# Performance work log

Hardware: AMD Instinct MI355X
Metric: run time of the kernel (lower is better)

## Reference

```python
import jax, jax.numpy as jnp
import numpy as np


def _cayley():
    """8x8x8 structure constants of Cl(3,0): (a*b)[r] = sum_pq a[p] b[q] C[p,q,r].
    Built by evaluating the original geometric_product formulas on basis one-hots."""
    C = np.zeros((8, 8, 8), dtype=np.float32)
    for p in range(8):
        a = np.zeros(8, dtype=np.float32); a[p] = 1.0
        for q in range(8):
            b = np.zeros(8, dtype=np.float32); b[q] = 1.0
            C[p, q] = [
                a[0]*b[0] + a[1]*b[1] + a[2]*b[2] + a[3]*b[3] - a[4]*b[4] - a[5]*b[5] - a[6]*b[6] - a[7]*b[7],
                a[0]*b[1] + a[1]*b[0] - a[2]*b[4] - a[3]*b[5] + a[4]*b[2] + a[5]*b[3] - a[6]*b[7] - a[7]*b[6],
                a[0]*b[2] + a[1]*b[4] + a[2]*b[0] - a[3]*b[6] - a[4]*b[1] + a[5]*b[7] + a[6]*b[3] + a[7]*b[5],
                a[0]*b[3] + a[1]*b[5] + a[2]*b[6] + a[3]*b[0] - a[4]*b[7] - a[5]*b[1] - a[6]*b[2] - a[7]*b[4],
                a[0]*b[4] + a[1]*b[2] - a[2]*b[1] + a[3]*b[7] + a[4]*b[0] - a[5]*b[6] + a[6]*b[5] + a[7]*b[3],
                a[0]*b[5] + a[1]*b[3] - a[2]*b[7] - a[3]*b[1] + a[4]*b[6] + a[5]*b[0] - a[6]*b[4] - a[7]*b[2],
                a[0]*b[6] + a[1]*b[7] + a[2]*b[3] - a[3]*b[2] - a[4]*b[5] + a[5]*b[4] + a[6]*b[0] + a[7]*b[1],
                a[0]*b[7] + a[1]*b[6] - a[2]*b[5] + a[3]*b[4] + a[4]*b[3] - a[5]*b[2] + a[6]*b[1] + a[7]*b[0],
            ]
    return C

_C = jnp.asarray(_cayley())  # [8,8,8]

BATCH, IN_F, OUT_F = 4096, 512, 512


def setup_inputs() -> dict:
    key = jax.random.key(0)
    k1, k2, k3 = jax.random.split(key, 3)
    return {
        "x": jax.random.normal(k1, (BATCH, IN_F, 8), dtype=jnp.float32),
        "weight": jax.random.normal(k2, (OUT_F, IN_F, 8), dtype=jnp.float32),
        "bias": jax.random.normal(k3, (OUT_F, 8), dtype=jnp.float32),
    }


def reference(x, weight, bias):
    # Precontract weight with Cayley table: Wc[i,j,p,r] = sum_q weight[i,j,q] C[p,q,r]
    Wc = jnp.einsum('ijq,pqr->ijpr', weight, _C)
    # out[b,i,r] = sum_{j,p} x[b,j,p] Wc[i,j,p,r]  (one big GEMM) + bias
    out = jnp.einsum('bjp,ijpr->bir', x, Wc) + bias[None, :, :]
    return out
```

## Files before the change

### kernel.cpp

```cpp
#include <hip/hip_runtime.h>
#include <hip/hip_bf16.h>


#define MDIM 4096
#define NDIM 4096
#define KDIM 4096
#define KTILES 64

typedef __attribute__((ext_vector_type(8))) __bf16 bf16x8;
typedef __attribute__((ext_vector_type(4))) float f32x4;
typedef __attribute__((ext_vector_type(8))) unsigned short ushort8;

__device__ __forceinline__ unsigned short f2bf(float f) {
  unsigned int u = __builtin_bit_cast(unsigned int, f);
  u += 0x7fffu + ((u >> 16) & 1u);
  return (unsigned short)(u >> 16);
}

__device__ const int QTAB[8][8] = {
  {0,1,2,3,4,5,6,7},
  {1,0,4,5,2,3,7,6},
  {2,4,0,6,1,7,3,5},
  {3,5,6,0,7,1,2,4},
  {4,2,1,7,0,6,5,3},
  {5,3,7,1,6,0,4,2},
  {6,7,3,2,5,4,0,1},
  {7,6,5,4,3,2,1,0},
};
__device__ const float STAB[8][8] = {
  { 1, 1, 1, 1,-1,-1,-1,-1},
  { 1, 1,-1,-1, 1, 1,-1,-1},
  { 1, 1, 1,-1,-1, 1, 1, 1},
  { 1, 1, 1, 1,-1,-1,-1,-1},
  { 1, 1,-1, 1, 1,-1, 1, 1},
  { 1, 1,-1,-1, 1, 1,-1,-1},
  { 1, 1, 1,-1,-1, 1, 1, 1},
  { 1, 1,-1, 1, 1,-1, 1, 1},
};

__global__ __launch_bounds__(256) void cast_x_kernel(
    const float* __restrict__ X, unsigned short* __restrict__ Xb) {
  const size_t t = (size_t)blockIdx.x * 256 + threadIdx.x;
  const float4* p = (const float4*)(X + t * 8);
  float4 a = p[0], b = p[1];
  ushort8 o;
  o[0] = f2bf(a.x); o[1] = f2bf(a.y); o[2] = f2bf(a.z); o[3] = f2bf(a.w);
  o[4] = f2bf(b.x); o[5] = f2bf(b.y); o[6] = f2bf(b.z); o[7] = f2bf(b.w);
  *(ushort8*)(Xb + t * 8) = o;
}

__global__ __launch_bounds__(256) void build_wc_kernel(
    const float* __restrict__ W, unsigned short* __restrict__ Wb) {
  const size_t t = (size_t)blockIdx.x * 256 + threadIdx.x;
  const int n = (int)(t >> 9);
  const int j = (int)(t & 511);
  const int i = n >> 3;
  const int r = n & 7;
  const float* wp = W + ((size_t)i * 512 + j) * 8;
  float4 w0 = *(const float4*)wp;
  float4 w1 = *(const float4*)(wp + 4);
  float w[8] = {w0.x, w0.y, w0.z, w0.w, w1.x, w1.y, w1.z, w1.w};
  ushort8 o;
#pragma unroll
  for (int p = 0; p < 8; ++p) o[p] = f2bf(STAB[r][p] * w[QTAB[r][p]]);
  *(ushort8*)(Wb + (size_t)n * KDIM + j * 8) = o;
}

typedef const __attribute__((address_space(1))) unsigned int as1_uint;
typedef __attribute__((address_space(3))) unsigned int as3_uint;

__device__ __forceinline__ void gload_lds16(const unsigned short* g,
                                            unsigned short* l) {
  __builtin_amdgcn_global_load_lds((as1_uint*)g, (as3_uint*)l, 16, 0, 0);
}

__device__ __forceinline__ void stage_half(
    const unsigned short* __restrict__ G, int gbase_row, int tile, int kh,
    unsigned short* lds_slot, int wid, int lane) {
#pragma unroll
  for (int q = 0; q < 2; ++q) {
    const int c = wid * 2 + q;
    const unsigned short* src = G
        + (size_t)(gbase_row + c * 16 + (lane >> 2)) * KDIM
        + tile * 64 + kh * 32 + (lane & 3) * 8;
    gload_lds16(src, lds_slot + c * 512);
  }
}

#define BAR()  asm volatile("s_barrier" ::: "memory")
#define VM6()  asm volatile("s_waitcnt vmcnt(6)" ::: "memory")
#define VM0()  asm volatile("s_waitcnt vmcnt(0)" ::: "memory")
#define NOSTAGE (void)0

#define PH(bufb, kk, mh, RDB, STAGE_STMT, VMC_STMT) do {                      \
    const unsigned short* As_ = &lds[(bufb)*4 + (kk)][0];                     \
    const unsigned short* Bs_ = &lds[(bufb)*4 + 2 + (kk)][0];                 \
    bf16x8 af[4];                                                             \
    _Pragma("unroll") for (int mi = 0; mi < 4; ++mi)                          \
      af[mi] = *(const bf16x8*)(As_ + (wm*128 + ((mh)*4+mi)*16 + fr)*32 + fq*8); \
    if (RDB) {                                                                \
      _Pragma("unroll") for (int n = 0; n < 4; ++n)                           \
        bfr[n] = *(const bf16x8*)(Bs_ + (wn*64 + n*16 + fr)*32 + fq*8);       \
    }                                                                         \
    STAGE_STMT;                                                               \
    VMC_STMT;                                                                 \
    BAR();                                                                    \
    __builtin_amdgcn_s_setprio(1);                                            \
    _Pragma("unroll") for (int mi = 0; mi < 4; ++mi)                          \
      _Pragma("unroll") for (int n = 0; n < 4; ++n)                           \
        acc[(mh)*4+mi][n] = __builtin_amdgcn_mfma_f32_16x16x32_bf16(          \
            af[mi], bfr[n], acc[(mh)*4+mi][n], 0, 0, 0);                      \
    __builtin_amdgcn_s_setprio(0);                                            \
    BAR();                                                                    \
  } while (0)

__global__ __launch_bounds__(512, 2) void gemm_bt_bias(
    const unsigned short* __restrict__ A,
    const unsigned short* __restrict__ B,
    const float* __restrict__ bias,
    float* __restrict__ C) {
  __shared__ unsigned short lds[8][8192];

  const int tid = threadIdx.x;
  const int wid = tid >> 6;
  const int lane = tid & 63;
  const int wm = wid >> 2;
  const int wn = wid & 3;
  const int fr = lane & 15;
  const int fq = lane >> 4;

  const int raw = blockIdx.x;
  const int wg = (raw & 7) * 32 + (raw >> 3);
  const int brow = (wg >> 4) * 256;
  const int bcol = (wg & 15) * 256;

  f32x4 acc[8][4];
#pragma unroll
  for (int m = 0; m < 8; ++m)
#pragma unroll
    for (int n = 0; n < 4; ++n) acc[m][n] = (f32x4){0.f, 0.f, 0.f, 0.f};
  bf16x8 bfr[4];

  stage_half(A, brow, 0, 0, &lds[0][0], wid, lane);
  stage_half(A, brow, 0, 1, &lds[1][0], wid, lane);
  stage_half(B, bcol, 0, 0, &lds[2][0], wid, lane);
  stage_half(B, bcol, 0, 1, &lds[3][0], wid, lane);
  stage_half(A, brow, 1, 0, &lds[4][0], wid, lane);
  stage_half(B, bcol, 1, 0, &lds[6][0], wid, lane);
  stage_half(B, bcol, 1, 1, &lds[7][0], wid, lane);
  VM6();
  BAR();

  for (int i = 0; i < KTILES / 2 - 1; ++i) {
    const int t0 = 2 * i, t1 = 2 * i + 1;
    PH(0, 0, 0, 1, stage_half(A, brow, t1,     1, &lds[5][0], wid, lane), NOSTAGE);
    PH(0, 0, 1, 0, stage_half(B, bcol, t0 + 2, 0, &lds[2][0], wid, lane), NOSTAGE);
    PH(0, 1, 0, 1, stage_half(A, brow, t0 + 2, 0, &lds[0][0], wid, lane), NOSTAGE);
    PH(0, 1, 1, 0, stage_half(B, bcol, t0 + 2, 1, &lds[3][0], wid, lane), VM6());
    PH(1, 0, 0, 1, stage_half(A, brow, t0 + 2, 1, &lds[1][0], wid, lane), NOSTAGE);
    PH(1, 0, 1, 0, stage_half(B, bcol, t1 + 2, 0, &lds[6][0], wid, lane), NOSTAGE);
    PH(1, 1, 0, 1, stage_half(A, brow, t1 + 2, 0, &lds[4][0], wid, lane), NOSTAGE);
    PH(1, 1, 1, 0, stage_half(B, bcol, t1 + 2, 1, &lds[7][0], wid, lane), VM6());
  }

  PH(0, 0, 0, 1, stage_half(A, brow, KTILES - 1, 1, &lds[5][0], wid, lane), NOSTAGE);
  PH(0, 0, 1, 0, NOSTAGE, NOSTAGE);
  PH(0, 1, 0, 1, NOSTAGE, NOSTAGE);
  PH(0, 1, 1, 0, NOSTAGE, VM0());
  PH(1, 0, 0, 1, NOSTAGE, NOSTAGE);
  PH(1, 0, 1, 0, NOSTAGE, NOSTAGE);
  PH(1, 1, 0, 1, NOSTAGE, NOSTAGE);
  PH(1, 1, 1, 0, NOSTAGE, NOSTAGE);

#pragma unroll
  for (int n = 0; n < 4; ++n) {
    const int col = bcol + wn * 64 + n * 16 + fr;
    const float bvs = bias[col];
#pragma unroll
    for (int m = 0; m < 8; ++m) {
      const int row0 = brow + wm * 128 + m * 16 + fq * 4;
#pragma unroll
      for (int j = 0; j < 4; ++j)
        C[(size_t)(row0 + j) * NDIM + col] = acc[m][n][j] + bvs;
    }
  }
}

extern "C" void kernel_launch(void* const* d_in, const int* in_sizes, int n_in,
                              void* d_out, int out_size, void* d_ws, size_t ws_size,
                              hipStream_t stream) {
  const float* x = (const float*)d_in[0];
  const float* w = (const float*)d_in[1];
  const float* bias = (const float*)d_in[2];
  float* out = (float*)d_out;

  unsigned short* Xb = (unsigned short*)d_ws;
  unsigned short* Wb = Xb + (size_t)MDIM * KDIM;

  cast_x_kernel<<<8192, 256, 0, stream>>>(x, Xb);
  build_wc_kernel<<<8192, 256, 0, stream>>>(w, Wb);
  gemm_bt_bias<<<256, 512, 0, stream>>>(Xb, Wb, bias, out);
}
```

Baseline: 259.0 us.

## Swizzle LDS column chunks to avoid bank conflicts and restructure Cayley weight build

The GEMM's global-to-LDS staging now XOR-swizzles the 16-byte column chunk within each 32-element row. The fragment reads apply the matching swizzle so ds_read_b128 accesses from different rows fall on different banks. The weight-expansion kernel now loads each weight element once, converts it to bf16 once, and emits all 8 permuted rows by sign-bit XOR. This replaces 8 redundant loads and per-element float multiplies, cutting the grid 8x. The risk is that the swizzle must match exactly between writer and reader.

```diff
diff --git a/kernel.cpp b/kernel.cpp
--- a/kernel.cpp
+++ b/kernel.cpp
@@ -17,7 +17,7 @@
   return (unsigned short)(u >> 16);
 }
 
-__device__ const int QTAB[8][8] = {
+static constexpr int QTAB[8][8] = {
   {0,1,2,3,4,5,6,7},
   {1,0,4,5,2,3,7,6},
   {2,4,0,6,1,7,3,5},
@@ -27,15 +27,15 @@
   {6,7,3,2,5,4,0,1},
   {7,6,5,4,3,2,1,0},
 };
-__device__ const float STAB[8][8] = {
-  { 1, 1, 1, 1,-1,-1,-1,-1},
-  { 1, 1,-1,-1, 1, 1,-1,-1},
-  { 1, 1, 1,-1,-1, 1, 1, 1},
-  { 1, 1, 1, 1,-1,-1,-1,-1},
-  { 1, 1,-1, 1, 1,-1, 1, 1},
-  { 1, 1,-1,-1, 1, 1,-1,-1},
-  { 1, 1, 1,-1,-1, 1, 1, 1},
-  { 1, 1,-1, 1, 1,-1, 1, 1},
+static constexpr unsigned short SBIT[8][8] = {
+  {0,0,0,0,0x8000,0x8000,0x8000,0x8000},
+  {0,0,0x8000,0x8000,0,0,0x8000,0x8000},
+  {0,0,0,0x8000,0x8000,0,0,0},
+  {0,0,0,0,0x8000,0x8000,0x8000,0x8000},
+  {0,0,0x8000,0,0,0x8000,0,0},
+  {0,0,0x8000,0x8000,0,0,0x8000,0x8000},
+  {0,0,0,0x8000,0x8000,0,0,0},
+  {0,0,0x8000,0,0,0x8000,0,0},
 };
 
 __global__ __launch_bounds__(256) void cast_x_kernel(
@@ -51,19 +51,21 @@
 
 __global__ __launch_bounds__(256) void build_wc_kernel(
     const float* __restrict__ W, unsigned short* __restrict__ Wb) {
-  const size_t t = (size_t)blockIdx.x * 256 + threadIdx.x;
-  const int n = (int)(t >> 9);
-  const int j = (int)(t & 511);
-  const int i = n >> 3;
-  const int r = n & 7;
-  const float* wp = W + ((size_t)i * 512 + j) * 8;
-  float4 w0 = *(const float4*)wp;
-  float4 w1 = *(const float4*)(wp + 4);
-  float w[8] = {w0.x, w0.y, w0.z, w0.w, w1.x, w1.y, w1.z, w1.w};
-  ushort8 o;
-#pragma unroll
-  for (int p = 0; p < 8; ++p) o[p] = f2bf(STAB[r][p] * w[QTAB[r][p]]);
-  *(ushort8*)(Wb + (size_t)n * KDIM + j * 8) = o;
+  const int t = blockIdx.x * 256 + threadIdx.x;
+  const int i = t >> 9;
+  const int j = t & 511;
+  const float4 w0 = *(const float4*)(W + (size_t)t * 8);
+  const float4 w1 = *(const float4*)(W + (size_t)t * 8 + 4);
+  const unsigned short b[8] = {f2bf(w0.x), f2bf(w0.y), f2bf(w0.z), f2bf(w0.w),
+                               f2bf(w1.x), f2bf(w1.y), f2bf(w1.z), f2bf(w1.w)};
+#pragma unroll
+  for (int r = 0; r < 8; ++r) {
+    ushort8 o;
+#pragma unroll
+    for (int p = 0; p < 8; ++p)
+      o[p] = (unsigned short)(b[QTAB[r][p]] ^ SBIT[r][p]);
+    *(ushort8*)(Wb + (size_t)(i * 8 + r) * KDIM + j * 8) = o;
+  }
 }
 
 typedef const __attribute__((address_space(1))) unsigned int as1_uint;
@@ -77,12 +79,13 @@
 __device__ __forceinline__ void stage_half(
     const unsigned short* __restrict__ G, int gbase_row, int tile, int kh,
     unsigned short* lds_slot, int wid, int lane) {
+  const int colswz = ((lane & 3) ^ ((lane >> 3) & 3)) * 8;
 #pragma unroll
   for (int q = 0; q < 2; ++q) {
     const int c = wid * 2 + q;
     const unsigned short* src = G
         + (size_t)(gbase_row + c * 16 + (lane >> 2)) * KDIM
-        + tile * 64 + kh * 32 + (lane & 3) * 8;
+        + tile * 64 + kh * 32 + colswz;
     gload_lds16(src, lds_slot + c * 512);
   }
 }
@@ -97,10 +100,10 @@
     const unsigned short* Bs_ = &lds[(bufb)*4 + 2 + (kk)][0];                 \
     bf16x8 af[4];                                                             \
     _Pragma("unroll") for (int mi = 0; mi < 4; ++mi)                          \
-      af[mi] = *(const bf16x8*)(As_ + (wm*128 + ((mh)*4+mi)*16 + fr)*32 + fq*8); \
+      af[mi] = *(const bf16x8*)(As_ + (wm*128 + ((mh)*4+mi)*16 + fr)*32 + fqs*8); \
     if (RDB) {                                                                \
       _Pragma("unroll") for (int n = 0; n < 4; ++n)                           \
-        bfr[n] = *(const bf16x8*)(Bs_ + (wn*64 + n*16 + fr)*32 + fq*8);       \
+        bfr[n] = *(const bf16x8*)(Bs_ + (wn*64 + n*16 + fr)*32 + fqs*8);      \
     }                                                                         \
     STAGE_STMT;                                                               \
     VMC_STMT;                                                                 \
@@ -128,6 +131,7 @@
   const int wn = wid & 3;
   const int fr = lane & 15;
   const int fq = lane >> 4;
+  const int fqs = fq ^ ((fr >> 1) & 3);
 
   const int raw = blockIdx.x;
   const int wg = (raw & 7) * 32 + (raw >> 3);
@@ -198,6 +202,6 @@
   unsigned short* Wb = Xb + (size_t)MDIM * KDIM;
 
   cast_x_kernel<<<8192, 256, 0, stream>>>(x, Xb);
-  build_wc_kernel<<<8192, 256, 0, stream>>>(w, Wb);
+  build_wc_kernel<<<1024, 256, 0, stream>>>(w, Wb);
   gemm_bt_bias<<<256, 512, 0, stream>>>(Xb, Wb, bias, out);
 }
```

After: 245.6 us. 5.2% less time.
